# Optimization experiments

Measured on AMD Instinct MI355X. Metric: run time of the kernel, lower is better.

The kernel has to match this reference:

```python
import jax, jax.numpy as jnp
import numpy as np

B, R, C, E, H = 2, 190, 512, 256, 8  # batch, pair-rows, alignment cols, embed, heads
D = E // H  # head_dim = 32; head_qk_dim = 1 since qk_dim == nb_heads


def setup_inputs() -> dict:
    key = jax.random.key(0)
    ks = jax.random.split(key, 6)
    s = 0.02
    return {
        "x": jax.random.normal(ks[0], (B, R, C, E), dtype=jnp.float32),
        "Wq": jax.random.normal(ks[1], (H, E), dtype=jnp.float32) * s,
        "bq": jnp.zeros((H,), dtype=jnp.float32),
        "Wk": jax.random.normal(ks[2], (H, E), dtype=jnp.float32) * s,
        "bk": jnp.zeros((H,), dtype=jnp.float32),
        "Wv": jax.random.normal(ks[3], (E, E), dtype=jnp.float32) * s,
        "bv": jnp.zeros((E,), dtype=jnp.float32),
        "Wo": jax.random.normal(ks[4], (E, E), dtype=jnp.float32) * s,
        "bo": jnp.zeros((E,), dtype=jnp.float32),
    }


def reference(x, Wq, bq, Wk, bk, Wv, bv, Wo, bo):
    b, r, c, e = x.shape
    h = Wq.shape[0]
    d = e // h
    # q,k projections: qk_dim == nb_heads, so per-head qk feature dim is 1.
    # Shapes: [b,r,h,c] (head axis before the col axis, matching transpose(2,3)).
    q = jnp.einsum('brce,he->brhc', x, Wq) + bq[:, None]
    k = jnp.einsum('brce,he->brhc', x, Wk) + bk[:, None]
    # v: [b,r,h,c,d]
    v = (jnp.einsum('brce,fe->brcf', x, Wv) + bv).reshape(b, r, c, h, d)
    v = jnp.transpose(v, (0, 1, 3, 2, 4))
    # elu+1 feature map, then normalize over the col (sequence) axis
    q = jax.nn.elu(q) + 1.0
    k = jax.nn.elu(k) + 1.0
    q = q / jnp.mean(q, axis=-1, keepdims=True)
    k = k / jnp.sum(k, axis=-1, keepdims=True)
    # KtV: k^T @ v with qk head-dim 1 -> [b,r,h,d]
    ktv = jnp.einsum('brhc,brhcd->brhd', k, v)
    # q @ KtV -> [b,r,c,h,d], flatten heads back to embed dim
    V = jnp.einsum('brhc,brhd->brchd', q, ktv).reshape(b, r, c, e)
    out = jnp.einsum('brce,fe->brcf', V, Wo) + bo
    return out
```

## Files before the change

kernel.cpp:

```cpp
#include <hip/hip_runtime.h>
#include <stdint.h>

#define PAIRS  380
#define CDIM   512
#define EDIM   256
#define HDIM   8
#define DDIM   32
#define CHUNK  64
#define NCHUNK 8
#define XSTR   260

__device__ __forceinline__ float bf2f(uint16_t u) {
  union { uint32_t i; float f; } v; v.i = ((uint32_t)u) << 16; return v.f;
}
__device__ __forceinline__ uint16_t f2bf(float f) {
  union { float f; uint32_t i; } v; v.f = f;
  return (uint16_t)((v.i + 0x7FFFu + ((v.i >> 16) & 1u)) >> 16);
}

__device__ __forceinline__ float4 ld4(const void* p, size_t idx, int f32) {
  if (f32) return ((const float4*)p)[idx >> 2];
  ushort4 u = *(const ushort4*)((const uint16_t*)p + idx);
  return make_float4(bf2f(u.x), bf2f(u.y), bf2f(u.z), bf2f(u.w));
}
__device__ __forceinline__ float ld1(const void* p, size_t idx, int f32) {
  return f32 ? ((const float*)p)[idx] : bf2f(((const uint16_t*)p)[idx]);
}

__global__ void sniff_all(const uint16_t* p0, const uint16_t* p1, const uint16_t* p2,
                          const uint16_t* p3, const uint16_t* p4, const uint16_t* p5,
                          const uint16_t* p6, const uint16_t* p7, const uint16_t* p8,
                          int n0, int n1, int n2, int n3, int n4, int n5, int n6,
                          int n7, int n8, int* __restrict__ flags) {
  const uint16_t* ps[9] = {p0, p1, p2, p3, p4, p5, p6, p7, p8};
  const int       ns[9] = {n0, n1, n2, n3, n4, n5, n6, n7, n8};
  __shared__ int sf;
  const int tid = threadIdx.x;
  #pragma unroll
  for (int j = 0; j < 9; ++j) {
    if (tid == 0) sf = 0;
    __syncthreads();
    const uint16_t* p = ps[j];
    int lim = ns[j] < 4096 ? ns[j] : 4096;
    int huge = 0;
    for (int i = tid; i < lim; i += 256) {
      int e = (p[i] >> 7) & 0xFF;
      huge |= (e >= 0xA0);
    }
    if (huge) atomicOr(&sf, 1);
    __syncthreads();
    if (tid == 0) flags[j] = sf;
    __syncthreads();
  }
}

__global__ void __launch_bounds__(256, 2)
sla_fused(const void* __restrict__ xg,
          const void* __restrict__ Wq, const void* __restrict__ bq,
          const void* __restrict__ Wk, const void* __restrict__ bk,
          const void* __restrict__ Wv, const void* __restrict__ bv,
          const void* __restrict__ Wo, const void* __restrict__ bo,
          const int* __restrict__ flags,
          float* __restrict__ outg)
{
  const int fx  = flags[0], fwq = flags[1], fbq = flags[2];
  const int fwk = flags[3], fbk = flags[4], fwv = flags[5];
  const int fbv = flags[6], fwo = flags[7], fbo = flags[8];

  __shared__ __align__(16) uint16_t xs[CHUNK][XSTR];
  __shared__ __align__(16) float    wqk[16][EDIM];
  __shared__ __align__(16) float    qv[CDIM][HDIM];
  __shared__ __align__(16) float    kc[CHUNK][HDIM];
  __shared__ __align__(16) float    ysh[HDIM][EDIM];
  __shared__ __align__(16) float    ktv[HDIM][DDIM];
  __shared__ __align__(16) float    scl[2][HDIM];

  const int tid  = threadIdx.x;
  const int pair = blockIdx.x;
  const size_t xbase = (size_t)pair * (CDIM * EDIM);

  for (int i = tid; i < 16 * EDIM / 4; i += 256) {
    int row = i >> 6;
    int col = (i & 63) << 2;
    float4 w = (row < 8) ? ld4(Wq, (size_t)row * EDIM + col, fwq)
                         : ld4(Wk, (size_t)(row - 8) * EDIM + col, fwk);
    *(float4*)&wqk[row][col] = w;
  }

  const int t  = tid >> 6;
  const int cl = tid & 63;
  const int h0 = (t & 1) * 4;
  const void* bsrc = (t < 2) ? bq : bk;
  const int   fb   = (t < 2) ? fbq : fbk;
  const float bias0 = ld1(bsrc, h0 + 0, fb), bias1 = ld1(bsrc, h0 + 1, fb),
              bias2 = ld1(bsrc, h0 + 2, fb), bias3 = ld1(bsrc, h0 + 3, fb);

  float yreg[HDIM] = {0.f,0.f,0.f,0.f,0.f,0.f,0.f,0.f};
  float cs0 = 0.f, cs1 = 0.f, cs2 = 0.f, cs3 = 0.f;

  for (int ch = 0; ch < NCHUNK; ++ch) {
    const int cbase = ch * CHUNK;
    __syncthreads();
    #pragma unroll
    for (int i = 0; i < 16; ++i) {
      int u  = i * 256 + tid;
      int c  = u >> 6;
      int e4 = (u & 63) << 2;
      float4 xv = ld4(xg, xbase + (size_t)(cbase + c) * EDIM + e4, fx);
      ushort4 s; s.x = f2bf(xv.x); s.y = f2bf(xv.y); s.z = f2bf(xv.z); s.w = f2bf(xv.w);
      *(ushort4*)&xs[c][e4] = s;
    }
    __syncthreads();
    {
      float a0 = bias0, a1 = bias1, a2 = bias2, a3 = bias3;
      const int r0 = t * 4;
      #pragma unroll 4
      for (int e = 0; e < EDIM; e += 4) {
        ushort4 xv = *(const ushort4*)&xs[cl][e];
        float x0 = bf2f(xv.x), x1 = bf2f(xv.y), x2 = bf2f(xv.z), x3 = bf2f(xv.w);
        float4 w0 = *(const float4*)&wqk[r0 + 0][e];
        float4 w1 = *(const float4*)&wqk[r0 + 1][e];
        float4 w2 = *(const float4*)&wqk[r0 + 2][e];
        float4 w3 = *(const float4*)&wqk[r0 + 3][e];
        a0 += x0 * w0.x + x1 * w0.y + x2 * w0.z + x3 * w0.w;
        a1 += x0 * w1.x + x1 * w1.y + x2 * w1.z + x3 * w1.w;
        a2 += x0 * w2.x + x1 * w2.y + x2 * w2.z + x3 * w2.w;
        a3 += x0 * w3.x + x1 * w3.y + x2 * w3.z + x3 * w3.w;
      }
      a0 = (a0 > 0.f) ? a0 + 1.f : __expf(a0);
      a1 = (a1 > 0.f) ? a1 + 1.f : __expf(a1);
      a2 = (a2 > 0.f) ? a2 + 1.f : __expf(a2);
      a3 = (a3 > 0.f) ? a3 + 1.f : __expf(a3);
      cs0 += a0; cs1 += a1; cs2 += a2; cs3 += a3;
      if (t < 2) *(float4*)&qv[cbase + cl][h0] = make_float4(a0, a1, a2, a3);
      else       *(float4*)&kc[cl][h0]        = make_float4(a0, a1, a2, a3);
    }
    __syncthreads();
    #pragma unroll 8
    for (int c = 0; c < CHUNK; ++c) {
      float xv = bf2f(xs[c][tid]);
      float4 k0 = *(const float4*)&kc[c][0];
      float4 k1 = *(const float4*)&kc[c][4];
      yreg[0] += k0.x * xv; yreg[1] += k0.y * xv; yreg[2] += k0.z * xv; yreg[3] += k0.w * xv;
      yreg[4] += k1.x * xv; yreg[5] += k1.y * xv; yreg[6] += k1.z * xv; yreg[7] += k1.w * xv;
    }
  }

  #pragma unroll
  for (int off = 32; off >= 1; off >>= 1) {
    cs0 += __shfl_xor(cs0, off, 64);
    cs1 += __shfl_xor(cs1, off, 64);
    cs2 += __shfl_xor(cs2, off, 64);
    cs3 += __shfl_xor(cs3, off, 64);
  }
  if ((tid & 63) == 0) {
    if (t < 2) *(float4*)&scl[0][h0] = make_float4(512.f / cs0, 512.f / cs1, 512.f / cs2, 512.f / cs3);
    else       *(float4*)&scl[1][h0] = make_float4(1.f / cs0, 1.f / cs1, 1.f / cs2, 1.f / cs3);
  }
  __syncthreads();

  {
    float4 k0 = *(const float4*)&scl[1][0];
    float4 k1 = *(const float4*)&scl[1][4];
    ysh[0][tid] = yreg[0] * k0.x; ysh[1][tid] = yreg[1] * k0.y;
    ysh[2][tid] = yreg[2] * k0.z; ysh[3][tid] = yreg[3] * k0.w;
    ysh[4][tid] = yreg[4] * k1.x; ysh[5][tid] = yreg[5] * k1.y;
    ysh[6][tid] = yreg[6] * k1.z; ysh[7][tid] = yreg[7] * k1.w;
  }
  __syncthreads();

  {
    const int h = tid >> 5, d = tid & 31;
    const size_t wvrow = (size_t)(h * DDIM + d) * EDIM;
    float acc = 0.f;
    #pragma unroll 4
    for (int e = 0; e < EDIM; e += 8) {
      float4 wa = ld4(Wv, wvrow + e, fwv);
      float4 wb = ld4(Wv, wvrow + e + 4, fwv);
      float4 ya = *(const float4*)&ysh[h][e];
      float4 yb = *(const float4*)&ysh[h][e + 4];
      acc += wa.x * ya.x + wa.y * ya.y + wa.z * ya.z + wa.w * ya.w
           + wb.x * yb.x + wb.y * yb.y + wb.z * yb.z + wb.w * yb.w;
    }
    ktv[h][d] = acc + ld1(bv, h * DDIM + d, fbv);
  }
  __syncthreads();

  float (*Msh)[EDIM] = (float (*)[EDIM])wqk;
  {
    const int f = tid;
    const size_t worow = (size_t)f * EDIM;
    #pragma unroll
    for (int h = 0; h < HDIM; ++h) {
      float m = 0.f;
      #pragma unroll
      for (int d = 0; d < DDIM; d += 8) {
        float4 wa = ld4(Wo, worow + h * DDIM + d, fwo);
        float4 wb = ld4(Wo, worow + h * DDIM + d + 4, fwo);
        float4 ka = *(const float4*)&ktv[h][d];
        float4 kb = *(const float4*)&ktv[h][d + 4];
        m += wa.x * ka.x + wa.y * ka.y + wa.z * ka.z + wa.w * ka.w
           + wb.x * kb.x + wb.y * kb.y + wb.z * kb.z + wb.w * kb.w;
      }
      Msh[h][f] = m * scl[0][h];
    }
  }
  __syncthreads();

  const int fq = tid & 63, cg = tid >> 6;
  const int f0 = fq * 4;
  float M[HDIM][4];
  #pragma unroll
  for (int h = 0; h < HDIM; ++h) {
    float4 mm = *(const float4*)&Msh[h][f0];
    M[h][0] = mm.x; M[h][1] = mm.y; M[h][2] = mm.z; M[h][3] = mm.w;
  }
  const float b0 = ld1(bo, f0 + 0, fbo), b1 = ld1(bo, f0 + 1, fbo),
              b2 = ld1(bo, f0 + 2, fbo), b3 = ld1(bo, f0 + 3, fbo);
  float* outp = outg + (size_t)pair * (CDIM * EDIM);
  for (int i = 0; i < 128; ++i) {
    int c = cg * 128 + i;
    float4 qa = *(const float4*)&qv[c][0];
    float4 qb = *(const float4*)&qv[c][4];
    float o0 = b0 + qa.x * M[0][0] + qa.y * M[1][0] + qa.z * M[2][0] + qa.w * M[3][0]
                  + qb.x * M[4][0] + qb.y * M[5][0] + qb.z * M[6][0] + qb.w * M[7][0];
    float o1 = b1 + qa.x * M[0][1] + qa.y * M[1][1] + qa.z * M[2][1] + qa.w * M[3][1]
                  + qb.x * M[4][1] + qb.y * M[5][1] + qb.z * M[6][1] + qb.w * M[7][1];
    float o2 = b2 + qa.x * M[0][2] + qa.y * M[1][2] + qa.z * M[2][2] + qa.w * M[3][2]
                  + qb.x * M[4][2] + qb.y * M[5][2] + qb.z * M[6][2] + qb.w * M[7][2];
    float o3 = b3 + qa.x * M[0][3] + qa.y * M[1][3] + qa.z * M[2][3] + qa.w * M[3][3]
                  + qb.x * M[4][3] + qb.y * M[5][3] + qb.z * M[6][3] + qb.w * M[7][3];
    *(float4*)(outp + (size_t)c * EDIM + f0) = make_float4(o0, o1, o2, o3);
  }
}

extern "C" void kernel_launch(void* const* d_in, const int* in_sizes, int n_in,
                              void* d_out, int out_size, void* d_ws, size_t ws_size,
                              hipStream_t stream) {
  (void)n_in; (void)out_size; (void)ws_size;
  int* flags = (int*)d_ws;
  hipLaunchKernelGGL(sniff_all, dim3(1), dim3(256), 0, stream,
                     (const uint16_t*)d_in[0], (const uint16_t*)d_in[1],
                     (const uint16_t*)d_in[2], (const uint16_t*)d_in[3],
                     (const uint16_t*)d_in[4], (const uint16_t*)d_in[5],
                     (const uint16_t*)d_in[6], (const uint16_t*)d_in[7],
                     (const uint16_t*)d_in[8],
                     in_sizes[0], in_sizes[1], in_sizes[2], in_sizes[3], in_sizes[4],
                     in_sizes[5], in_sizes[6], in_sizes[7], in_sizes[8], flags);
  hipLaunchKernelGGL(sla_fused, dim3(PAIRS), dim3(256), 0, stream,
                     d_in[0], d_in[1], d_in[2], d_in[3], d_in[4],
                     d_in[5], d_in[6], d_in[7], d_in[8], (const int*)flags,
                     (float*)d_out);
}
```

Before: 516.7 us.

## Split fused kernel into three phases to raise block-level parallelism

Replaces the single 380-block fused kernel with three launches. Phase 1 splits each pair's column chunks across 4 blocks and writes q values, partial column sums and partial k^T x into scratch. Phase 2 reduces the partials and computes the per-pair output matrix. Phase 3 writes the output across 4 column segments per pair. The aim is to fill more CUs than 380 blocks can on a 256-CU device, at the cost of extra launches and scratch global-memory traffic. When the workspace is too small, the output buffer is reused as scratch.

```diff
diff --git a/kernel.cpp b/kernel.cpp
--- a/kernel.cpp
+++ b/kernel.cpp
@@ -9,6 +9,16 @@
 #define CHUNK  64
 #define NCHUNK 8
 #define XSTR   260
+#define NSPLIT 4
+#define CPS    2
+
+#define Q_OFF      0
+#define MSH_OFF    4096
+#define YP_OFF     6144
+#define QS_OFF     14336
+#define KS_OFF     14368
+#define SCR_FLOATS 14400
+#define OUT_STRIDE 131072
 
 __device__ __forceinline__ float bf2f(uint16_t u) {
   union { uint32_t i; float f; } v; v.i = ((uint32_t)u) << 16; return v.f;
@@ -55,29 +65,24 @@
 }
 
 __global__ void __launch_bounds__(256, 2)
-sla_fused(const void* __restrict__ xg,
-          const void* __restrict__ Wq, const void* __restrict__ bq,
-          const void* __restrict__ Wk, const void* __restrict__ bk,
-          const void* __restrict__ Wv, const void* __restrict__ bv,
-          const void* __restrict__ Wo, const void* __restrict__ bo,
-          const int* __restrict__ flags,
-          float* __restrict__ outg)
+sla_phase1(const void* __restrict__ xg,
+           const void* __restrict__ Wq, const void* __restrict__ bq,
+           const void* __restrict__ Wk, const void* __restrict__ bk,
+           const int* __restrict__ flags,
+           float* __restrict__ scratch, long long sstride)
 {
-  const int fx  = flags[0], fwq = flags[1], fbq = flags[2];
-  const int fwk = flags[3], fbk = flags[4], fwv = flags[5];
-  const int fbv = flags[6], fwo = flags[7], fbo = flags[8];
+  const int fx = flags[0], fwq = flags[1], fbq = flags[2];
+  const int fwk = flags[3], fbk = flags[4];
 
   __shared__ __align__(16) uint16_t xs[CHUNK][XSTR];
   __shared__ __align__(16) float    wqk[16][EDIM];
-  __shared__ __align__(16) float    qv[CDIM][HDIM];
   __shared__ __align__(16) float    kc[CHUNK][HDIM];
-  __shared__ __align__(16) float    ysh[HDIM][EDIM];
-  __shared__ __align__(16) float    ktv[HDIM][DDIM];
-  __shared__ __align__(16) float    scl[2][HDIM];
 
   const int tid  = threadIdx.x;
-  const int pair = blockIdx.x;
+  const int pair = blockIdx.x / NSPLIT;
+  const int sp   = blockIdx.x % NSPLIT;
   const size_t xbase = (size_t)pair * (CDIM * EDIM);
+  float* sbase = scratch + (size_t)pair * (size_t)sstride;
 
   for (int i = tid; i < 16 * EDIM / 4; i += 256) {
     int row = i >> 6;
@@ -98,8 +103,8 @@
   float yreg[HDIM] = {0.f,0.f,0.f,0.f,0.f,0.f,0.f,0.f};
   float cs0 = 0.f, cs1 = 0.f, cs2 = 0.f, cs3 = 0.f;
 
-  for (int ch = 0; ch < NCHUNK; ++ch) {
-    const int cbase = ch * CHUNK;
+  for (int ci = 0; ci < CPS; ++ci) {
+    const int cbase = (sp * CPS + ci) * CHUNK;
     __syncthreads();
     #pragma unroll
     for (int i = 0; i < 16; ++i) {
@@ -132,8 +137,9 @@
       a2 = (a2 > 0.f) ? a2 + 1.f : __expf(a2);
       a3 = (a3 > 0.f) ? a3 + 1.f : __expf(a3);
       cs0 += a0; cs1 += a1; cs2 += a2; cs3 += a3;
-      if (t < 2) *(float4*)&qv[cbase + cl][h0] = make_float4(a0, a1, a2, a3);
-      else       *(float4*)&kc[cl][h0]        = make_float4(a0, a1, a2, a3);
+      if (t < 2) *(float4*)&sbase[Q_OFF + (size_t)(cbase + cl) * HDIM + h0]
+                   = make_float4(a0, a1, a2, a3);
+      else       *(float4*)&kc[cl][h0] = make_float4(a0, a1, a2, a3);
     }
     __syncthreads();
     #pragma unroll 8
@@ -154,18 +160,48 @@
     cs3 += __shfl_xor(cs3, off, 64);
   }
   if ((tid & 63) == 0) {
-    if (t < 2) *(float4*)&scl[0][h0] = make_float4(512.f / cs0, 512.f / cs1, 512.f / cs2, 512.f / cs3);
-    else       *(float4*)&scl[1][h0] = make_float4(1.f / cs0, 1.f / cs1, 1.f / cs2, 1.f / cs3);
+    if (t < 2) *(float4*)&sbase[QS_OFF + sp * HDIM + h0] = make_float4(cs0, cs1, cs2, cs3);
+    else       *(float4*)&sbase[KS_OFF + sp * HDIM + h0] = make_float4(cs0, cs1, cs2, cs3);
+  }
+
+  float* yp = sbase + YP_OFF + (size_t)sp * (HDIM * EDIM);
+  #pragma unroll
+  for (int h = 0; h < HDIM; ++h) yp[h * EDIM + tid] = yreg[h];
+}
+
+__global__ void __launch_bounds__(256, 2)
+sla_phase2(const void* __restrict__ Wv, const void* __restrict__ bv,
+           const void* __restrict__ Wo,
+           const int* __restrict__ flags,
+           float* __restrict__ scratch, long long sstride)
+{
+  const int fwv = flags[5], fbv = flags[6], fwo = flags[7];
+  __shared__ __align__(16) float ysh[HDIM][EDIM];
+  __shared__ __align__(16) float ktv[HDIM][DDIM];
+  __shared__ float sQ[HDIM], sK[HDIM];
+  const int tid = threadIdx.x;
+  float* sbase = scratch + (size_t)blockIdx.x * (size_t)sstride;
+
+  if (tid < 16) {
+    int h = tid & 7;
+    const float* ps = sbase + ((tid < 8) ? QS_OFF : KS_OFF);
+    float s = 0.f;
+    #pragma unroll
+    for (int sp = 0; sp < NSPLIT; ++sp) s += ps[sp * HDIM + h];
+    if (tid < 8) sQ[h] = 512.f / s;
+    else         sK[h] = 1.f / s;
   }
   __syncthreads();
 
   {
-    float4 k0 = *(const float4*)&scl[1][0];
-    float4 k1 = *(const float4*)&scl[1][4];
-    ysh[0][tid] = yreg[0] * k0.x; ysh[1][tid] = yreg[1] * k0.y;
-    ysh[2][tid] = yreg[2] * k0.z; ysh[3][tid] = yreg[3] * k0.w;
-    ysh[4][tid] = yreg[4] * k1.x; ysh[5][tid] = yreg[5] * k1.y;
-    ysh[6][tid] = yreg[6] * k1.z; ysh[7][tid] = yreg[7] * k1.w;
+    const float* yp = sbase + YP_OFF;
+    #pragma unroll
+    for (int h = 0; h < HDIM; ++h) {
+      float y = 0.f;
+      #pragma unroll
+      for (int sp = 0; sp < NSPLIT; ++sp) y += yp[(sp * HDIM + h) * EDIM + tid];
+      ysh[h][tid] = y * sK[h];
+    }
   }
   __syncthreads();
 
@@ -186,10 +222,10 @@
   }
   __syncthreads();
 
-  float (*Msh)[EDIM] = (float (*)[EDIM])wqk;
   {
     const int f = tid;
     const size_t worow = (size_t)f * EDIM;
+    float* msh = sbase + MSH_OFF;
     #pragma unroll
     for (int h = 0; h < HDIM; ++h) {
       float m = 0.f;
@@ -202,7 +238,34 @@
         m += wa.x * ka.x + wa.y * ka.y + wa.z * ka.z + wa.w * ka.w
            + wb.x * kb.x + wb.y * kb.y + wb.z * kb.z + wb.w * kb.w;
       }
-      Msh[h][f] = m * scl[0][h];
+      msh[h * EDIM + f] = m * sQ[h];
+    }
+  }
+}
+
+__global__ void __launch_bounds__(256, 2)
+sla_phase3(const float* __restrict__ scratch, long long sstride,
+           const void* __restrict__ bo, const int* __restrict__ flags,
+           float* __restrict__ outg, int shift)
+{
+  const int fbo = flags[8];
+  __shared__ __align__(16) float qsh[CDIM][HDIM];
+  __shared__ __align__(16) float msh[HDIM][EDIM];
+  const int tid  = threadIdx.x;
+  const int pair = blockIdx.x >> shift;
+  const int seg  = blockIdx.x & ((1 << shift) - 1);
+  const int rows = CDIM >> shift;
+  const int c0   = seg * rows;
+  const float* sbase = scratch + (size_t)pair * (size_t)sstride;
+
+  for (int i = tid; i < rows * HDIM / 4; i += 256) {
+    *(float4*)&qsh[i >> 1][(i & 1) * 4] =
+        *(const float4*)&sbase[Q_OFF + (size_t)c0 * HDIM + (size_t)i * 4];
+  }
+  {
+    const float* mp = sbase + MSH_OFF;
+    for (int i = tid; i < HDIM * EDIM / 4; i += 256) {
+      *(float4*)((float*)msh + (size_t)i * 4) = *(const float4*)&mp[(size_t)i * 4];
     }
   }
   __syncthreads();
@@ -212,16 +275,17 @@
   float M[HDIM][4];
   #pragma unroll
   for (int h = 0; h < HDIM; ++h) {
-    float4 mm = *(const float4*)&Msh[h][f0];
+    float4 mm = *(const float4*)&msh[h][f0];
     M[h][0] = mm.x; M[h][1] = mm.y; M[h][2] = mm.z; M[h][3] = mm.w;
   }
   const float b0 = ld1(bo, f0 + 0, fbo), b1 = ld1(bo, f0 + 1, fbo),
               b2 = ld1(bo, f0 + 2, fbo), b3 = ld1(bo, f0 + 3, fbo);
-  float* outp = outg + (size_t)pair * (CDIM * EDIM);
-  for (int i = 0; i < 128; ++i) {
-    int c = cg * 128 + i;
-    float4 qa = *(const float4*)&qv[c][0];
-    float4 qb = *(const float4*)&qv[c][4];
+  float* outp = outg + (size_t)pair * OUT_STRIDE;
+  const int rpw = rows >> 2;
+  for (int i = 0; i < rpw; ++i) {
+    int c = cg * rpw + i;
+    float4 qa = *(const float4*)&qsh[c][0];
+    float4 qb = *(const float4*)&qsh[c][4];
     float o0 = b0 + qa.x * M[0][0] + qa.y * M[1][0] + qa.z * M[2][0] + qa.w * M[3][0]
                   + qb.x * M[4][0] + qb.y * M[5][0] + qb.z * M[6][0] + qb.w * M[7][0];
     float o1 = b1 + qa.x * M[0][1] + qa.y * M[1][1] + qa.z * M[2][1] + qa.w * M[3][1]
@@ -230,14 +294,14 @@
                   + qb.x * M[4][2] + qb.y * M[5][2] + qb.z * M[6][2] + qb.w * M[7][2];
     float o3 = b3 + qa.x * M[0][3] + qa.y * M[1][3] + qa.z * M[2][3] + qa.w * M[3][3]
                   + qb.x * M[4][3] + qb.y * M[5][3] + qb.z * M[6][3] + qb.w * M[7][3];
-    *(float4*)(outp + (size_t)c * EDIM + f0) = make_float4(o0, o1, o2, o3);
+    *(float4*)(outp + (size_t)(c0 + c) * EDIM + f0) = make_float4(o0, o1, o2, o3);
   }
 }
 
 extern "C" void kernel_launch(void* const* d_in, const int* in_sizes, int n_in,
                               void* d_out, int out_size, void* d_ws, size_t ws_size,
                               hipStream_t stream) {
-  (void)n_in; (void)out_size; (void)ws_size;
+  (void)n_in; (void)out_size;
   int* flags = (int*)d_ws;
   hipLaunchKernelGGL(sniff_all, dim3(1), dim3(256), 0, stream,
                      (const uint16_t*)d_in[0], (const uint16_t*)d_in[1],
@@ -247,8 +311,27 @@
                      (const uint16_t*)d_in[8],
                      in_sizes[0], in_sizes[1], in_sizes[2], in_sizes[3], in_sizes[4],
                      in_sizes[5], in_sizes[6], in_sizes[7], in_sizes[8], flags);
-  hipLaunchKernelGGL(sla_fused, dim3(PAIRS), dim3(256), 0, stream,
+
+  const size_t need = 256 + (size_t)PAIRS * SCR_FLOATS * sizeof(float);
+  float*    scratch;
+  long long sstride;
+  int       shift;
+  if (ws_size >= need) {
+    scratch = (float*)((char*)d_ws + 256);
+    sstride = SCR_FLOATS;
+    shift   = 2;
+  } else {
+    scratch = (float*)d_out;
+    sstride = OUT_STRIDE;
+    shift   = 0;
+  }
+
+  hipLaunchKernelGGL(sla_phase1, dim3(PAIRS * NSPLIT), dim3(256), 0, stream,
                      d_in[0], d_in[1], d_in[2], d_in[3], d_in[4],
-                     d_in[5], d_in[6], d_in[7], d_in[8], (const int*)flags,
-                     (float*)d_out);
-}
+                     (const int*)flags, scratch, sstride);
+  hipLaunchKernelGGL(sla_phase2, dim3(PAIRS), dim3(256), 0, stream,
+                     d_in[5], d_in[6], d_in[7], (const int*)flags, scratch, sstride);
+  hipLaunchKernelGGL(sla_phase3, dim3(PAIRS << shift), dim3(256), 0, stream,
+                     scratch, sstride, d_in[8], (const int*)flags,
+                     (float*)d_out, shift);
+}
```

Result: faster. 482.1 us (-6.7%).
